# Kernel tuning notes

Hardware: AMD Instinct MI355X
Metric: run time of the kernel (lower is better)

## Reference

```python
import jax, jax.numpy as jnp
import numpy as np
from math import sqrt

D_MODEL = 512
HEADS = 8
D_K = D_MODEL // HEADS
DIM_FFN = 2048
EPS = 1e-6


def setup_inputs() -> dict:
    key = jax.random.key(0)
    ks = jax.random.split(key, 16)
    b, s = 2, 256
    inp = {
        "x": jax.random.normal(ks[0], (b, s, D_MODEL), dtype=jnp.float32),
        "connection_bias_k": jax.random.normal(ks[1], (b, s, s, D_MODEL), dtype=jnp.float32) * 0.02,
        "connection_bias_v": jax.random.normal(ks[2], (b, s, s, D_MODEL), dtype=jnp.float32) * 0.02,
        "mask": jnp.zeros((b, s), dtype=jnp.int32),
        "Wq": jax.random.normal(ks[3], (D_MODEL, D_MODEL), dtype=jnp.float32) / sqrt(D_MODEL),
        "bq": jnp.zeros((D_MODEL,), dtype=jnp.float32),
        "Wk": jax.random.normal(ks[4], (D_MODEL, D_MODEL), dtype=jnp.float32) / sqrt(D_MODEL),
        "bk": jnp.zeros((D_MODEL,), dtype=jnp.float32),
        "Wv": jax.random.normal(ks[5], (D_MODEL, D_MODEL), dtype=jnp.float32) / sqrt(D_MODEL),
        "bv": jnp.zeros((D_MODEL,), dtype=jnp.float32),
        "Wo": jax.random.normal(ks[6], (D_MODEL, D_MODEL), dtype=jnp.float32) / sqrt(D_MODEL),
        "bo": jnp.zeros((D_MODEL,), dtype=jnp.float32),
        "alpha1": jnp.ones((D_MODEL,), dtype=jnp.float32),
        "beta1": jnp.zeros((D_MODEL,), dtype=jnp.float32),
        "alpha2": jnp.ones((D_MODEL,), dtype=jnp.float32),
        "beta2": jnp.zeros((D_MODEL,), dtype=jnp.float32),
        "W1": jax.random.normal(ks[7], (DIM_FFN, D_MODEL), dtype=jnp.float32) / sqrt(D_MODEL),
        "b1": jnp.zeros((DIM_FFN,), dtype=jnp.float32),
        "W2": jax.random.normal(ks[8], (D_MODEL, DIM_FFN), dtype=jnp.float32) / sqrt(DIM_FFN),
        "b2": jnp.zeros((D_MODEL,), dtype=jnp.float32),
    }
    return inp


def _norm(x, alpha, beta):
    # torch .std() is unbiased (ddof=1); note std is added to eps OUTSIDE variance
    mu = jnp.mean(x, axis=-1, keepdims=True)
    sd = jnp.std(x, axis=-1, ddof=1, keepdims=True)
    return alpha * (x - mu) / (sd + EPS) + beta


def reference(x, connection_bias_k, connection_bias_v, mask,
              Wq, bq, Wk, bk, Wv, bv, Wo, bo,
              alpha1, beta1, alpha2, beta2, W1, b1, W2, b2):
    b, s, _ = x.shape
    h, dk = HEADS, D_K

    x2 = _norm(x, alpha1, beta1)
    # projections -> [b, h, s, dk]
    q = (x2 @ Wq.T + bq).reshape(b, s, h, dk).transpose(0, 2, 1, 3)
    k = (x2 @ Wk.T + bk).reshape(b, s, h, dk).transpose(0, 2, 1, 3)
    v = (x2 @ Wv.T + bv).reshape(b, s, h, dk).transpose(0, 2, 1, 3)

    # biases reshaped to (b, s1, s2, h, dk); biased_k[b,h,i,j] = k[b,h,j] + bias[b,j,i,h]
    bk_r = connection_bias_k.reshape(b, s, s, h, dk)
    bv_r = connection_bias_v.reshape(b, s, s, h, dk)

    # scores[b,h,i,j] = q_i . (k_j + bias_k[b,j,i,h]) / sqrt(dk)
    scores = (jnp.einsum('bhid,bhjd->bhij', q, k)
              + jnp.einsum('bhid,bjihd->bhij', q, bk_r)) / sqrt(dk)

    # mask [b,s] -> [b,1,s,1], broadcast over heads and key dim (matches torch)
    m = mask[:, None, :, None]
    scores = jnp.where(m == 1, -1e9, scores)
    attn = jax.nn.softmax(scores, axis=-1)

    # out[b,h,i,d] = sum_j attn[b,h,i,j] * (v[b,h,j] + bias_v[b,j,i,h])
    out = (jnp.einsum('bhij,bhjd->bhid', attn, v)
           + jnp.einsum('bhij,bjihd->bhid', attn, bv_r))
    concat = out.transpose(0, 2, 1, 3).reshape(b, s, D_MODEL)
    attn_out = concat @ Wo.T + bo

    x = x + attn_out
    x2 = _norm(x, alpha2, beta2)
    ff = jax.nn.relu(x2 @ W1.T + b1) @ W2.T + b2
    return x + ff
```

## Files before the change

### kernel.cpp

```cpp
#include <hip/hip_runtime.h>
#include <math.h>

#define D_MODEL 512
#define NHEADS 8
#define DK 64
#define DFFN 2048

typedef __attribute__((ext_vector_type(8))) __bf16 bf16x8;
typedef __attribute__((ext_vector_type(4))) float floatx4;

__global__ __launch_bounds__(256) void ln_kernel(
    const float* __restrict__ x, const float* __restrict__ alpha,
    const float* __restrict__ beta, __bf16* __restrict__ y) {
  int row = blockIdx.x;
  int t = threadIdx.x;
  const float* xr = x + (size_t)row * D_MODEL;
  float2 v = ((const float2*)xr)[t];
  __shared__ float rs[256], rq[256];
  rs[t] = v.x + v.y;
  rq[t] = v.x * v.x + v.y * v.y;
  __syncthreads();
  for (int o = 128; o > 0; o >>= 1) {
    if (t < o) { rs[t] += rs[t + o]; rq[t] += rq[t + o]; }
    __syncthreads();
  }
  float mu = rs[0] * (1.0f / D_MODEL);
  float var = (rq[0] - (float)D_MODEL * mu * mu) * (1.0f / (D_MODEL - 1));
  float inv = 1.0f / (sqrtf(fmaxf(var, 0.0f)) + 1e-6f);
  float2 a2 = ((const float2*)alpha)[t];
  float2 b2 = ((const float2*)beta)[t];
  union { __bf16 h2[2]; unsigned int u; } pk;
  pk.h2[0] = (__bf16)(a2.x * (v.x - mu) * inv + b2.x);
  pk.h2[1] = (__bf16)(a2.y * (v.y - mu) * inv + b2.y);
  *(unsigned int*)(y + (size_t)row * D_MODEL + 2 * t) = pk.u;
}

struct Seg { const float* src; __bf16* dst; int n4; };
struct Segs6 { Seg s[6]; };
__global__ __launch_bounds__(256) void cast6(Segs6 cs) {
  Seg sg = cs.s[blockIdx.y];
  int stride = gridDim.x * 256;
  for (int idx = blockIdx.x * 256 + threadIdx.x; idx < sg.n4; idx += stride) {
    float4 f = ((const float4*)sg.src)[idx];
    union { __bf16 h[4]; uint2 u; } pk;
    pk.h[0] = (__bf16)f.x; pk.h[1] = (__bf16)f.y;
    pk.h[2] = (__bf16)f.z; pk.h[3] = (__bf16)f.w;
    ((uint2*)sg.dst)[idx] = pk.u;
  }
}

__global__ __launch_bounds__(256) void pack_bias(
    const float* __restrict__ bq, const float* __restrict__ bk,
    const float* __restrict__ bv, float* __restrict__ dst) {
  int idx = blockIdx.x * 256 + threadIdx.x;
  if (idx >= 3 * D_MODEL) return;
  float v = idx < 512 ? bq[idx] : (idx < 1024 ? bk[idx - 512] : bv[idx - 1024]);
  dst[idx] = v;
}

template <int RELU, int OUT_BF16>
__global__ __launch_bounds__(64) void wave_gemm(
    const __bf16* __restrict__ A, int lda, const __bf16* __restrict__ B, int ldb,
    const float* __restrict__ bias, const float* __restrict__ res,
    void* __restrict__ Cv, int N, int K) {
  int lane = threadIdx.x;
  int r16 = lane & 15;
  int ko = (lane >> 4) * 8;
  int m0 = blockIdx.y * 32, n0 = blockIdx.x * 32;
  const __bf16* A0 = A + (size_t)(m0 + r16) * lda + ko;
  const __bf16* A1 = A0 + (size_t)16 * lda;
  const __bf16* B0 = B + (size_t)(n0 + r16) * ldb + ko;
  const __bf16* B1 = B0 + (size_t)16 * ldb;
  floatx4 acc00 = {0.f, 0.f, 0.f, 0.f};
  floatx4 acc01 = acc00, acc10 = acc00, acc11 = acc00;
#pragma unroll 4
  for (int k0 = 0; k0 < K; k0 += 32) {
    bf16x8 a0 = *(const bf16x8*)(A0 + k0);
    bf16x8 a1 = *(const bf16x8*)(A1 + k0);
    bf16x8 b0 = *(const bf16x8*)(B0 + k0);
    bf16x8 b1 = *(const bf16x8*)(B1 + k0);
    acc00 = __builtin_amdgcn_mfma_f32_16x16x32_bf16(a0, b0, acc00, 0, 0, 0);
    acc01 = __builtin_amdgcn_mfma_f32_16x16x32_bf16(a0, b1, acc01, 0, 0, 0);
    acc10 = __builtin_amdgcn_mfma_f32_16x16x32_bf16(a1, b0, acc10, 0, 0, 0);
    acc11 = __builtin_amdgcn_mfma_f32_16x16x32_bf16(a1, b1, acc11, 0, 0, 0);
  }
  int col = lane & 15, rb = (lane >> 4) * 4;
  floatx4 accs[2][2] = {{acc00, acc01}, {acc10, acc11}};
#pragma unroll
  for (int i = 0; i < 2; ++i) {
#pragma unroll
    for (int j = 0; j < 2; ++j) {
#pragma unroll
      for (int r = 0; r < 4; ++r) {
        int row = m0 + i * 16 + rb + r;
        int cc = n0 + j * 16 + col;
        float v = accs[i][j][r] + bias[cc];
        if (res) v += res[(size_t)row * N + cc];
        if (RELU) v = fmaxf(v, 0.0f);
        if (OUT_BF16)
          ((__bf16*)Cv)[(size_t)row * N + cc] = (__bf16)v;
        else
          ((float*)Cv)[(size_t)row * N + cc] = v;
      }
    }
  }
}

__global__ __launch_bounds__(256) void attn_scores(
    const float* __restrict__ qkv, int ldq, const float* __restrict__ cbk,
    float* __restrict__ sc_out, int s) {
  int jb = blockIdx.x;
  int i = blockIdx.y;
  int b = blockIdx.z;
  int t = threadIdx.x;
  int w = t >> 6, lane = t & 63, h = lane >> 3;
  __shared__ float scl[64][9];
  size_t tok_i = (size_t)(b * s + i);
  const float* qp = qkv + tok_i * ldq + lane * 8;
  float4 q0 = *(const float4*)qp;
  float4 q1 = *(const float4*)(qp + 4);
  int jbase = jb * 64 + w * 16;
#pragma unroll 4
  for (int jj = 0; jj < 16; ++jj) {
    int j = jbase + jj;
    size_t tok_j = (size_t)(b * s + j);
    const float* kp = qkv + tok_j * ldq + 512 + lane * 8;
    const float* cp = cbk + (tok_j * s + i) * (size_t)D_MODEL + lane * 8;
    float4 k0 = *(const float4*)kp;
    float4 k1 = *(const float4*)(kp + 4);
    float4 c0 = *(const float4*)cp;
    float4 c1 = *(const float4*)(cp + 4);
    float d = q0.x * (k0.x + c0.x) + q0.y * (k0.y + c0.y) +
              q0.z * (k0.z + c0.z) + q0.w * (k0.w + c0.w) +
              q1.x * (k1.x + c1.x) + q1.y * (k1.y + c1.y) +
              q1.z * (k1.z + c1.z) + q1.w * (k1.w + c1.w);
    d += __shfl_xor(d, 1);
    d += __shfl_xor(d, 2);
    d += __shfl_xor(d, 4);
    if ((lane & 7) == 0) scl[w * 16 + jj][h] = d * 0.125f;
  }
  __syncthreads();
  int hh = t >> 5;
  int jj2 = (t & 31) * 2;
  float2 v2;
  v2.x = scl[jj2][hh];
  v2.y = scl[jj2 + 1][hh];
  *(float2*)(sc_out + (tok_i * NHEADS + hh) * s + jb * 64 + jj2) = v2;
}

__global__ __launch_bounds__(256) void attn_softmax(
    float* __restrict__ sc, const int* __restrict__ mask, int s) {
  int row = blockIdx.x * 4 + (threadIdx.x >> 6);
  int lane = threadIdx.x & 63;
  float* p = sc + (size_t)row * s;
  float4 v = ((float4*)p)[lane];
  if (mask[row >> 3] == 1) { v.x = -1e9f; v.y = -1e9f; v.z = -1e9f; v.w = -1e9f; }
  float mx = fmaxf(fmaxf(v.x, v.y), fmaxf(v.z, v.w));
  for (int m = 1; m < 64; m <<= 1) mx = fmaxf(mx, __shfl_xor(mx, m));
  float e0 = expf(v.x - mx), e1 = expf(v.y - mx);
  float e2 = expf(v.z - mx), e3 = expf(v.w - mx);
  float ls = e0 + e1 + e2 + e3;
  for (int m = 1; m < 64; m <<= 1) ls += __shfl_xor(ls, m);
  float inv = 1.0f / ls;
  float4 o = {e0 * inv, e1 * inv, e2 * inv, e3 * inv};
  ((float4*)p)[lane] = o;
}

__global__ __launch_bounds__(256) void attn_pv(
    const float* __restrict__ qkv, int ldq, const float* __restrict__ cbv,
    const float* __restrict__ p, float* __restrict__ part, int s) {
  int jb = blockIdx.x;
  int i = blockIdx.y;
  int b = blockIdx.z;
  int t = threadIdx.x;
  int w = t >> 6, lane = t & 63, h = lane >> 3;
  __shared__ float pl[NHEADS][64];
  __shared__ float accs[4][D_MODEL];
  size_t tok_i = (size_t)(b * s + i);
  {
    int hh = t >> 5;
    int jj2 = (t & 31) * 2;
    float2 pv = *(const float2*)(p + (tok_i * NHEADS + hh) * s + jb * 64 + jj2);
    pl[hh][jj2] = pv.x;
    pl[hh][jj2 + 1] = pv.y;
  }
  __syncthreads();
  float4 a0 = {0.f, 0.f, 0.f, 0.f};
  float4 a1 = {0.f, 0.f, 0.f, 0.f};
  int jbase = jb * 64 + w * 16;
#pragma unroll 4
  for (int jj = 0; jj < 16; ++jj) {
    int j = jbase + jj;
    size_t tok_j = (size_t)(b * s + j);
    const float* vp = qkv + tok_j * ldq + 1024 + lane * 8;
    const float* cp = cbv + (tok_j * s + i) * (size_t)D_MODEL + lane * 8;
    float4 v0 = *(const float4*)vp;
    float4 v1 = *(const float4*)(vp + 4);
    float4 c0 = *(const float4*)cp;
    float4 c1 = *(const float4*)(cp + 4);
    float pj = pl[h][w * 16 + jj];
    a0.x += pj * (v0.x + c0.x); a0.y += pj * (v0.y + c0.y);
    a0.z += pj * (v0.z + c0.z); a0.w += pj * (v0.w + c0.w);
    a1.x += pj * (v1.x + c1.x); a1.y += pj * (v1.y + c1.y);
    a1.z += pj * (v1.z + c1.z); a1.w += pj * (v1.w + c1.w);
  }
  *(float4*)&accs[w][lane * 8] = a0;
  *(float4*)&accs[w][lane * 8 + 4] = a1;
  __syncthreads();
  int d0 = t * 2;
  float2 o;
  o.x = accs[0][d0] + accs[1][d0] + accs[2][d0] + accs[3][d0];
  o.y = accs[0][d0 + 1] + accs[1][d0 + 1] + accs[2][d0 + 1] + accs[3][d0 + 1];
  *(float2*)(part + (tok_i * 4 + jb) * (size_t)D_MODEL + d0) = o;
}

__global__ __launch_bounds__(256) void attn_reduce(
    const float* __restrict__ part, __bf16* __restrict__ concat) {
  size_t tok = blockIdx.x;
  int d0 = threadIdx.x * 2;
  const float* pp = part + tok * 4 * D_MODEL + d0;
  float2 v0 = *(const float2*)(pp);
  float2 v1 = *(const float2*)(pp + D_MODEL);
  float2 v2 = *(const float2*)(pp + 2 * D_MODEL);
  float2 v3 = *(const float2*)(pp + 3 * D_MODEL);
  union { __bf16 h2[2]; unsigned int u; } pk;
  pk.h2[0] = (__bf16)(v0.x + v1.x + v2.x + v3.x);
  pk.h2[1] = (__bf16)(v0.y + v1.y + v2.y + v3.y);
  *(unsigned int*)(concat + tok * D_MODEL + d0) = pk.u;
}

extern "C" void kernel_launch(void* const* d_in, const int* in_sizes, int n_in,
                              void* d_out, int out_size, void* d_ws, size_t ws_size,
                              hipStream_t stream) {
  const float* x      = (const float*)d_in[0];
  const float* cbk    = (const float*)d_in[1];
  const float* cbv    = (const float*)d_in[2];
  const int*   mask   = (const int*)d_in[3];
  const float* Wq     = (const float*)d_in[4];
  const float* bq     = (const float*)d_in[5];
  const float* Wk     = (const float*)d_in[6];
  const float* bk     = (const float*)d_in[7];
  const float* Wv     = (const float*)d_in[8];
  const float* bv     = (const float*)d_in[9];
  const float* Wo     = (const float*)d_in[10];
  const float* bo     = (const float*)d_in[11];
  const float* alpha1 = (const float*)d_in[12];
  const float* beta1  = (const float*)d_in[13];
  const float* alpha2 = (const float*)d_in[14];
  const float* beta2  = (const float*)d_in[15];
  const float* W1     = (const float*)d_in[16];
  const float* b1     = (const float*)d_in[17];
  const float* W2     = (const float*)d_in[18];
  const float* b2     = (const float*)d_in[19];

  int bs = in_sizes[0] / D_MODEL;
  int s  = in_sizes[1] / in_sizes[0];
  int b  = bs / s;

  char* wp = (char*)d_ws;
  auto carve = [&](size_t bytes) {
    char* p = wp;
    wp += (bytes + 255) & ~(size_t)255;
    return p;
  };
  __bf16* x2    = (__bf16*)carve((size_t)bs * D_MODEL * 2);
  __bf16* wqkv  = (__bf16*)carve((size_t)3 * D_MODEL * D_MODEL * 2);
  __bf16* wo_b  = (__bf16*)carve((size_t)D_MODEL * D_MODEL * 2);
  __bf16* w1_b  = (__bf16*)carve((size_t)DFFN * D_MODEL * 2);
  __bf16* w2_b  = (__bf16*)carve((size_t)D_MODEL * DFFN * 2);
  float*  bqkv  = (float*)carve((size_t)3 * D_MODEL * 4);
  float*  qkv   = (float*)carve((size_t)bs * 3 * D_MODEL * 4);
  float*  sc_ws = (float*)carve((size_t)bs * NHEADS * s * 4);
  float*  partw = (float*)carve((size_t)bs * 4 * D_MODEL * 4);
  __bf16* conc  = (__bf16*)carve((size_t)bs * D_MODEL * 2);
  float*  xres  = (float*)carve((size_t)bs * D_MODEL * 4);
  __bf16* x2b   = (__bf16*)carve((size_t)bs * D_MODEL * 2);
  __bf16* f1    = (__bf16*)carve((size_t)bs * DFFN * 2);

  Segs6 cs;
  cs.s[0] = {Wq, wqkv,                         D_MODEL * D_MODEL / 4};
  cs.s[1] = {Wk, wqkv + D_MODEL * D_MODEL,     D_MODEL * D_MODEL / 4};
  cs.s[2] = {Wv, wqkv + 2 * D_MODEL * D_MODEL, D_MODEL * D_MODEL / 4};
  cs.s[3] = {Wo, wo_b, D_MODEL * D_MODEL / 4};
  cs.s[4] = {W1, w1_b, DFFN * D_MODEL / 4};
  cs.s[5] = {W2, w2_b, D_MODEL * DFFN / 4};
  cast6<<<dim3(256, 6), 256, 0, stream>>>(cs);
  pack_bias<<<6, 256, 0, stream>>>(bq, bk, bv, bqkv);

  ln_kernel<<<bs, 256, 0, stream>>>(x, alpha1, beta1, x2);

  wave_gemm<0, 0><<<dim3(3 * D_MODEL / 32, bs / 32), 64, 0, stream>>>(
      x2, D_MODEL, wqkv, D_MODEL, bqkv, nullptr, qkv, 3 * D_MODEL, D_MODEL);

  attn_scores<<<dim3(4, s, b), 256, 0, stream>>>(qkv, 3 * D_MODEL, cbk, sc_ws, s);
  attn_softmax<<<bs * NHEADS / 4, 256, 0, stream>>>(sc_ws, mask, s);
  attn_pv<<<dim3(4, s, b), 256, 0, stream>>>(qkv, 3 * D_MODEL, cbv, sc_ws, partw, s);
  attn_reduce<<<bs, 256, 0, stream>>>(partw, conc);

  wave_gemm<0, 0><<<dim3(D_MODEL / 32, bs / 32), 64, 0, stream>>>(
      conc, D_MODEL, wo_b, D_MODEL, bo, x, xres, D_MODEL, D_MODEL);

  ln_kernel<<<bs, 256, 0, stream>>>(xres, alpha2, beta2, x2b);

  wave_gemm<1, 1><<<dim3(DFFN / 32, bs / 32), 64, 0, stream>>>(
      x2b, D_MODEL, w1_b, D_MODEL, b1, nullptr, f1, DFFN, D_MODEL);

  wave_gemm<0, 0><<<dim3(D_MODEL / 32, bs / 32), 64, 0, stream>>>(
      f1, DFFN, w2_b, DFFN, b2, xres, d_out, D_MODEL, DFFN);
}
```

Measured before the change: 633.5 us.

## Fuse softmax into score/PV kernels, fold bias packing into GEMM, use nontemporal loads

Removes the separate softmax kernel. The score kernel now applies the mask and writes per-block max/sum statistics, and the PV kernel merges those partial statistics and exponentiates the scores on the fly. The pack_bias launch is dropped by selecting among the q/k/v biases inside the QKV GEMM epilogue. The large connection-bias streams are read with nontemporal loads to reduce cache pollution. Together these cut two launches and one pass over the score buffer, at the cost of recomputing exp in the PV kernel.

```diff
diff --git a/kernel.cpp b/kernel.cpp
--- a/kernel.cpp
+++ b/kernel.cpp
@@ -8,6 +8,11 @@
 
 typedef __attribute__((ext_vector_type(8))) __bf16 bf16x8;
 typedef __attribute__((ext_vector_type(4))) float floatx4;
+
+static __device__ inline float4 ntload4(const float* p) {
+  floatx4 v = __builtin_nontemporal_load((const floatx4*)p);
+  return make_float4(v.x, v.y, v.z, v.w);
+}
 
 __global__ __launch_bounds__(256) void ln_kernel(
     const float* __restrict__ x, const float* __restrict__ alpha,
@@ -49,19 +54,11 @@
   }
 }
 
-__global__ __launch_bounds__(256) void pack_bias(
-    const float* __restrict__ bq, const float* __restrict__ bk,
-    const float* __restrict__ bv, float* __restrict__ dst) {
-  int idx = blockIdx.x * 256 + threadIdx.x;
-  if (idx >= 3 * D_MODEL) return;
-  float v = idx < 512 ? bq[idx] : (idx < 1024 ? bk[idx - 512] : bv[idx - 1024]);
-  dst[idx] = v;
-}
-
-template <int RELU, int OUT_BF16>
+template <int RELU, int OUT_BF16, int BIAS3>
 __global__ __launch_bounds__(64) void wave_gemm(
     const __bf16* __restrict__ A, int lda, const __bf16* __restrict__ B, int ldb,
-    const float* __restrict__ bias, const float* __restrict__ res,
+    const float* __restrict__ bias, const float* __restrict__ bias2,
+    const float* __restrict__ bias3, const float* __restrict__ res,
     void* __restrict__ Cv, int N, int K) {
   int lane = threadIdx.x;
   int r16 = lane & 15;
@@ -90,11 +87,16 @@
   for (int i = 0; i < 2; ++i) {
 #pragma unroll
     for (int j = 0; j < 2; ++j) {
+      int cc = n0 + j * 16 + col;
+      float bv_;
+      if (BIAS3)
+        bv_ = cc < 512 ? bias[cc] : (cc < 1024 ? bias2[cc - 512] : bias3[cc - 1024]);
+      else
+        bv_ = bias[cc];
 #pragma unroll
       for (int r = 0; r < 4; ++r) {
         int row = m0 + i * 16 + rb + r;
-        int cc = n0 + j * 16 + col;
-        float v = accs[i][j][r] + bias[cc];
+        float v = accs[i][j][r] + bv_;
         if (res) v += res[(size_t)row * N + cc];
         if (RELU) v = fmaxf(v, 0.0f);
         if (OUT_BF16)
@@ -108,7 +110,8 @@
 
 __global__ __launch_bounds__(256) void attn_scores(
     const float* __restrict__ qkv, int ldq, const float* __restrict__ cbk,
-    float* __restrict__ sc_out, int s) {
+    const int* __restrict__ mask, float* __restrict__ sc_out,
+    float2* __restrict__ stats, int s) {
   int jb = blockIdx.x;
   int i = blockIdx.y;
   int b = blockIdx.z;
@@ -128,8 +131,8 @@
     const float* cp = cbk + (tok_j * s + i) * (size_t)D_MODEL + lane * 8;
     float4 k0 = *(const float4*)kp;
     float4 k1 = *(const float4*)(kp + 4);
-    float4 c0 = *(const float4*)cp;
-    float4 c1 = *(const float4*)(cp + 4);
+    float4 c0 = ntload4(cp);
+    float4 c1 = ntload4(cp + 4);
     float d = q0.x * (k0.x + c0.x) + q0.y * (k0.y + c0.y) +
               q0.z * (k0.z + c0.z) + q0.w * (k0.w + c0.w) +
               q1.x * (k1.x + c1.x) + q1.y * (k1.y + c1.y) +
@@ -142,47 +145,54 @@
   __syncthreads();
   int hh = t >> 5;
   int jj2 = (t & 31) * 2;
-  float2 v2;
-  v2.x = scl[jj2][hh];
-  v2.y = scl[jj2 + 1][hh];
+  bool masked = (mask[b * s + i] == 1);
+  float v0 = masked ? -1e9f : scl[jj2][hh];
+  float v1 = masked ? -1e9f : scl[jj2 + 1][hh];
+  float2 v2 = {v0, v1};
   *(float2*)(sc_out + (tok_i * NHEADS + hh) * s + jb * 64 + jj2) = v2;
-}
-
-__global__ __launch_bounds__(256) void attn_softmax(
-    float* __restrict__ sc, const int* __restrict__ mask, int s) {
-  int row = blockIdx.x * 4 + (threadIdx.x >> 6);
-  int lane = threadIdx.x & 63;
-  float* p = sc + (size_t)row * s;
-  float4 v = ((float4*)p)[lane];
-  if (mask[row >> 3] == 1) { v.x = -1e9f; v.y = -1e9f; v.z = -1e9f; v.w = -1e9f; }
-  float mx = fmaxf(fmaxf(v.x, v.y), fmaxf(v.z, v.w));
-  for (int m = 1; m < 64; m <<= 1) mx = fmaxf(mx, __shfl_xor(mx, m));
-  float e0 = expf(v.x - mx), e1 = expf(v.y - mx);
-  float e2 = expf(v.z - mx), e3 = expf(v.w - mx);
-  float ls = e0 + e1 + e2 + e3;
-  for (int m = 1; m < 64; m <<= 1) ls += __shfl_xor(ls, m);
-  float inv = 1.0f / ls;
-  float4 o = {e0 * inv, e1 * inv, e2 * inv, e3 * inv};
-  ((float4*)p)[lane] = o;
+  float mx = fmaxf(v0, v1);
+  for (int m = 1; m < 32; m <<= 1) mx = fmaxf(mx, __shfl_xor(mx, m, 32));
+  float se = expf(v0 - mx) + expf(v1 - mx);
+  for (int m = 1; m < 32; m <<= 1) se += __shfl_xor(se, m, 32);
+  if ((t & 31) == 0) {
+    float2 st = {mx, se};
+    stats[(tok_i * NHEADS + hh) * 4 + jb] = st;
+  }
 }
 
 __global__ __launch_bounds__(256) void attn_pv(
     const float* __restrict__ qkv, int ldq, const float* __restrict__ cbv,
-    const float* __restrict__ p, float* __restrict__ part, int s) {
+    const float* __restrict__ sc, const float2* __restrict__ stats,
+    float* __restrict__ part, int s) {
   int jb = blockIdx.x;
   int i = blockIdx.y;
   int b = blockIdx.z;
   int t = threadIdx.x;
   int w = t >> 6, lane = t & 63, h = lane >> 3;
+  __shared__ float2 sst[NHEADS][4];
+  __shared__ float sM[NHEADS], sInvS[NHEADS];
   __shared__ float pl[NHEADS][64];
   __shared__ float accs[4][D_MODEL];
   size_t tok_i = (size_t)(b * s + i);
+  if (t < 32) sst[t >> 2][t & 3] = stats[(tok_i * NHEADS + (t >> 2)) * 4 + (t & 3)];
+  __syncthreads();
+  if (t < NHEADS) {
+    float M = -1e30f;
+#pragma unroll
+    for (int q = 0; q < 4; ++q) M = fmaxf(M, sst[t][q].x);
+    float S = 0.f;
+#pragma unroll
+    for (int q = 0; q < 4; ++q) S += sst[t][q].y * expf(sst[t][q].x - M);
+    sM[t] = M;
+    sInvS[t] = 1.0f / S;
+  }
+  __syncthreads();
   {
     int hh = t >> 5;
     int jj2 = (t & 31) * 2;
-    float2 pv = *(const float2*)(p + (tok_i * NHEADS + hh) * s + jb * 64 + jj2);
-    pl[hh][jj2] = pv.x;
-    pl[hh][jj2 + 1] = pv.y;
+    float2 sv = *(const float2*)(sc + (tok_i * NHEADS + hh) * s + jb * 64 + jj2);
+    pl[hh][jj2]     = expf(sv.x - sM[hh]) * sInvS[hh];
+    pl[hh][jj2 + 1] = expf(sv.y - sM[hh]) * sInvS[hh];
   }
   __syncthreads();
   float4 a0 = {0.f, 0.f, 0.f, 0.f};
@@ -196,8 +206,8 @@
     const float* cp = cbv + (tok_j * s + i) * (size_t)D_MODEL + lane * 8;
     float4 v0 = *(const float4*)vp;
     float4 v1 = *(const float4*)(vp + 4);
-    float4 c0 = *(const float4*)cp;
-    float4 c1 = *(const float4*)(cp + 4);
+    float4 c0 = ntload4(cp);
+    float4 c1 = ntload4(cp + 4);
     float pj = pl[h][w * 16 + jj];
     a0.x += pj * (v0.x + c0.x); a0.y += pj * (v0.y + c0.y);
     a0.z += pj * (v0.z + c0.z); a0.w += pj * (v0.w + c0.w);
@@ -268,9 +278,9 @@
   __bf16* wo_b  = (__bf16*)carve((size_t)D_MODEL * D_MODEL * 2);
   __bf16* w1_b  = (__bf16*)carve((size_t)DFFN * D_MODEL * 2);
   __bf16* w2_b  = (__bf16*)carve((size_t)D_MODEL * DFFN * 2);
-  float*  bqkv  = (float*)carve((size_t)3 * D_MODEL * 4);
   float*  qkv   = (float*)carve((size_t)bs * 3 * D_MODEL * 4);
   float*  sc_ws = (float*)carve((size_t)bs * NHEADS * s * 4);
+  float2* stats = (float2*)carve((size_t)bs * NHEADS * 4 * 8);
   float*  partw = (float*)carve((size_t)bs * 4 * D_MODEL * 4);
   __bf16* conc  = (__bf16*)carve((size_t)bs * D_MODEL * 2);
   float*  xres  = (float*)carve((size_t)bs * D_MODEL * 4);
@@ -285,26 +295,26 @@
   cs.s[4] = {W1, w1_b, DFFN * D_MODEL / 4};
   cs.s[5] = {W2, w2_b, D_MODEL * DFFN / 4};
   cast6<<<dim3(256, 6), 256, 0, stream>>>(cs);
-  pack_bias<<<6, 256, 0, stream>>>(bq, bk, bv, bqkv);
 
   ln_kernel<<<bs, 256, 0, stream>>>(x, alpha1, beta1, x2);
 
-  wave_gemm<0, 0><<<dim3(3 * D_MODEL / 32, bs / 32), 64, 0, stream>>>(
-      x2, D_MODEL, wqkv, D_MODEL, bqkv, nullptr, qkv, 3 * D_MODEL, D_MODEL);
-
-  attn_scores<<<dim3(4, s, b), 256, 0, stream>>>(qkv, 3 * D_MODEL, cbk, sc_ws, s);
-  attn_softmax<<<bs * NHEADS / 4, 256, 0, stream>>>(sc_ws, mask, s);
-  attn_pv<<<dim3(4, s, b), 256, 0, stream>>>(qkv, 3 * D_MODEL, cbv, sc_ws, partw, s);
+  wave_gemm<0, 0, 1><<<dim3(3 * D_MODEL / 32, bs / 32), 64, 0, stream>>>(
+      x2, D_MODEL, wqkv, D_MODEL, bq, bk, bv, nullptr, qkv, 3 * D_MODEL, D_MODEL);
+
+  attn_scores<<<dim3(4, s, b), 256, 0, stream>>>(qkv, 3 * D_MODEL, cbk, mask,
+                                                 sc_ws, stats, s);
+  attn_pv<<<dim3(4, s, b), 256, 0, stream>>>(qkv, 3 * D_MODEL, cbv, sc_ws,
+                                             stats, partw, s);
   attn_reduce<<<bs, 256, 0, stream>>>(partw, conc);
 
-  wave_gemm<0, 0><<<dim3(D_MODEL / 32, bs / 32), 64, 0, stream>>>(
-      conc, D_MODEL, wo_b, D_MODEL, bo, x, xres, D_MODEL, D_MODEL);
+  wave_gemm<0, 0, 0><<<dim3(D_MODEL / 32, bs / 32), 64, 0, stream>>>(
+      conc, D_MODEL, wo_b, D_MODEL, bo, nullptr, nullptr, x, xres, D_MODEL, D_MODEL);
 
   ln_kernel<<<bs, 256, 0, stream>>>(xres, alpha2, beta2, x2b);
 
-  wave_gemm<1, 1><<<dim3(DFFN / 32, bs / 32), 64, 0, stream>>>(
-      x2b, D_MODEL, w1_b, D_MODEL, b1, nullptr, f1, DFFN, D_MODEL);
-
-  wave_gemm<0, 0><<<dim3(D_MODEL / 32, bs / 32), 64, 0, stream>>>(
-      f1, DFFN, w2_b, DFFN, b2, xres, d_out, D_MODEL, DFFN);
-}
+  wave_gemm<1, 1, 0><<<dim3(DFFN / 32, bs / 32), 64, 0, stream>>>(
+      x2b, D_MODEL, w1_b, D_MODEL, b1, nullptr, nullptr, nullptr, f1, DFFN, D_MODEL);
+
+  wave_gemm<0, 0, 0><<<dim3(D_MODEL / 32, bs / 32), 64, 0, stream>>>(
+      f1, DFFN, w2_b, DFFN, b2, nullptr, nullptr, xres, d_out, D_MODEL, DFFN);
+}
```

New measurement: 629.0 us. No clear change (-0.7%).
